# Performance work log

Measured on AMD Instinct MI355X. Metric: run time of the kernel, lower is better.

Reference implementation:

```python
import jax, jax.numpy as jnp
import numpy as np

B, S, D = 16, 2048, 768  # batch, padded subword length, roberta hidden dim


def setup_inputs() -> dict:
    key = jax.random.key(0)
    k1, k2 = jax.random.split(key)
    robert_embed = jax.random.normal(k1, (B, S, D), dtype=jnp.float32)
    # Non-decreasing per-row segment ids: contiguous runs of equal ids are the
    # subword spans that merge_list would average; singleton runs pass through.
    seg_ids = jnp.sort(jax.random.randint(k2, (B, S), 0, S, dtype=jnp.int32), axis=-1)
    return {"robert_embed": robert_embed, "seg_ids": seg_ids}


def reference(robert_embed, seg_ids):
    # Segment-mean gather/scatter: out[b, w] = mean_{p: seg_ids[b,p]==w} x[b, p]
    b, s, d = robert_embed.shape
    w = s  # output word slots (<= s); empty slots yield zeros
    flat_seg = (seg_ids + (w * jnp.arange(b, dtype=seg_ids.dtype))[:, None]).reshape(-1)
    x_flat = robert_embed.reshape(-1, d)
    sums = jax.ops.segment_sum(x_flat, flat_seg, num_segments=b * w)  # [b*w, d]
    counts = jax.ops.segment_sum(
        jnp.ones((b * s,), dtype=robert_embed.dtype), flat_seg, num_segments=b * w
    )
    out = sums / jnp.maximum(counts, 1)[:, None]
    return out.reshape(b, w, d)
```

## Files before the change

kernel.cpp:

```cpp
#include <hip/hip_runtime.h>

#define BB 16
#define SS 2048
#define DD 768
#define D4 (DD / 4)
#define SPB 16
#define BLOCKS_PER_ROW (SS / SPB)

typedef float vfloat4 __attribute__((ext_vector_type(4)));

__global__ __launch_bounds__(256) void seg_mean_v3(
    const float* __restrict__ x,
    const int*   __restrict__ seg,
    float*       __restrict__ out) {
    __shared__ int sLb[SPB + 1];

    int b  = blockIdx.x >> 7;
    int w0 = (blockIdx.x & (BLOCKS_PER_ROW - 1)) << 4;
    const int* srow = seg + (b << 11);

    if (threadIdx.x <= SPB) {
        int w  = w0 + threadIdx.x;
        int lo = 0, n = SS;
        while (n > 0) {
            int half = n >> 1;
            int mid  = lo + half;
            if (srow[mid] < w) { lo = mid + 1; n -= half + 1; }
            else               { n = half; }
        }
        sLb[threadIdx.x] = lo;
    }
    __syncthreads();

    int lane = threadIdx.x & 63;
    int wave = threadIdx.x >> 6;
    size_t rowBase = (size_t)(b << 11);

    for (int si = (wave << 2); si < (wave << 2) + 4; ++si) {
        int st = sLb[si];
        int c  = sLb[si + 1] - st;
        vfloat4* outp = (vfloat4*)(out + (rowBase + (size_t)(w0 + si)) * DD);

        if (c == 0) {
            vfloat4 z = (vfloat4){0.f, 0.f, 0.f, 0.f};
            __builtin_nontemporal_store(z, &outp[lane]);
            __builtin_nontemporal_store(z, &outp[lane + 64]);
            __builtin_nontemporal_store(z, &outp[lane + 128]);
            continue;
        }

        const vfloat4* xp = (const vfloat4*)(x + (rowBase + (size_t)st) * DD);
        vfloat4 a0 = xp[lane];
        vfloat4 a1 = xp[lane + 64];
        vfloat4 a2 = xp[lane + 128];
        for (int j = 1; j < c; ++j) {
            const vfloat4* xr = xp + (size_t)j * D4;
            a0 += xr[lane];
            a1 += xr[lane + 64];
            a2 += xr[lane + 128];
        }
        float inv = 1.0f / (float)c;
        a0 *= inv;
        a1 *= inv;
        a2 *= inv;
        __builtin_nontemporal_store(a0, &outp[lane]);
        __builtin_nontemporal_store(a1, &outp[lane + 64]);
        __builtin_nontemporal_store(a2, &outp[lane + 128]);
    }
}

extern "C" void kernel_launch(void* const* d_in, const int* in_sizes, int n_in,
                              void* d_out, int out_size, void* d_ws, size_t ws_size,
                              hipStream_t stream) {
    const float* x   = (const float*)d_in[0];
    const int*   seg = (const int*)d_in[1];
    float* out = (float*)d_out;

    int nBlocks = BB * BLOCKS_PER_ROW;
    seg_mean_v3<<<nBlocks, 256, 0, stream>>>(x, seg, out);
}
```

Baseline: 185.3 us.

## Stream input positions per block with register prefetch instead of per-output binary search

Switches from output-slot partitioning, where each block binary-searches segment bounds, to input-position partitioning. Each 192-thread block loads the full segment row into shared memory, owns 16 input positions, and walks runs that start in its chunk. It keeps an 8-deep register prefetch of input rows and writes the means plus zero-fill for empty slots in between. This is meant to remove serial dependent loads and global binary searches and to keep more loads in flight. The cost is copying the whole 2048-entry seg row per block, a serial scan with divergent branches, and uneven work when long runs or long zero gaps fall on one block.

```diff
diff --git a/kernel.cpp b/kernel.cpp
--- a/kernel.cpp
+++ b/kernel.cpp
@@ -3,70 +3,101 @@
 #define BB 16
 #define SS 2048
 #define DD 768
-#define D4 (DD / 4)
-#define SPB 16
-#define BLOCKS_PER_ROW (SS / SPB)
+#define D4 192
+#define P  16
+#define CPR (SS / P)
+#define PF 8
+#define NT 192
 
 typedef float vfloat4 __attribute__((ext_vector_type(4)));
 
-__global__ __launch_bounds__(256) void seg_mean_v3(
+__global__ __launch_bounds__(NT) void seg_mean_stream(
     const float* __restrict__ x,
     const int*   __restrict__ seg,
-    float*       __restrict__ out) {
-    __shared__ int sLb[SPB + 1];
+    float*       __restrict__ out)
+{
+    __shared__ __align__(16) int sseg[SS];
 
-    int b  = blockIdx.x >> 7;
-    int w0 = (blockIdx.x & (BLOCKS_PER_ROW - 1)) << 4;
-    const int* srow = seg + (b << 11);
+    const int b     = blockIdx.x >> 7;
+    const int chunk = blockIdx.x & (CPR - 1);
+    const int p0 = chunk * P;
+    const int p1 = p0 + P;
+    const int t  = threadIdx.x;
 
-    if (threadIdx.x <= SPB) {
-        int w  = w0 + threadIdx.x;
-        int lo = 0, n = SS;
-        while (n > 0) {
-            int half = n >> 1;
-            int mid  = lo + half;
-            if (srow[mid] < w) { lo = mid + 1; n -= half + 1; }
-            else               { n = half; }
+    {
+        const int4* s4 = (const int4*)(seg + (b << 11));
+        int4* l4 = (int4*)sseg;
+        #pragma unroll
+        for (int i = 0; i < 3; ++i) {
+            int idx = t + i * NT;
+            if (idx < SS / 4) l4[idx] = s4[idx];
         }
-        sLb[threadIdx.x] = lo;
     }
     __syncthreads();
 
-    int lane = threadIdx.x & 63;
-    int wave = threadIdx.x >> 6;
-    size_t rowBase = (size_t)(b << 11);
+    const int prev = (p0 == 0) ? -1 : sseg[p0 - 1];
+    int p = p0;
+    while (p < p1 && sseg[p] == prev) ++p;
+    if (p >= p1) return;
 
-    for (int si = (wave << 2); si < (wave << 2) + 4; ++si) {
-        int st = sLb[si];
-        int c  = sLb[si + 1] - st;
-        vfloat4* outp = (vfloat4*)(out + (rowBase + (size_t)(w0 + si)) * DD);
+    int pe = p1;
+    while (pe < SS && sseg[pe] == sseg[pe - 1]) ++pe;
 
-        if (c == 0) {
-            vfloat4 z = (vfloat4){0.f, 0.f, 0.f, 0.f};
-            __builtin_nontemporal_store(z, &outp[lane]);
-            __builtin_nontemporal_store(z, &outp[lane + 64]);
-            __builtin_nontemporal_store(z, &outp[lane + 128]);
-            continue;
-        }
+    const vfloat4* xrow = (const vfloat4*)(x + (((size_t)b) << 11) * DD);
+    float* outrow = out + (((size_t)b) << 11) * DD;
+    const vfloat4 z = (vfloat4){0.f, 0.f, 0.f, 0.f};
 
-        const vfloat4* xp = (const vfloat4*)(x + (rowBase + (size_t)st) * DD);
-        vfloat4 a0 = xp[lane];
-        vfloat4 a1 = xp[lane + 64];
-        vfloat4 a2 = xp[lane + 128];
-        for (int j = 1; j < c; ++j) {
-            const vfloat4* xr = xp + (size_t)j * D4;
-            a0 += xr[lane];
-            a1 += xr[lane + 64];
-            a2 += xr[lane + 128];
-        }
-        float inv = 1.0f / (float)c;
-        a0 *= inv;
-        a1 *= inv;
-        a2 *= inv;
-        __builtin_nontemporal_store(a0, &outp[lane]);
-        __builtin_nontemporal_store(a1, &outp[lane + 64]);
-        __builtin_nontemporal_store(a2, &outp[lane + 128]);
+    int runid = sseg[p];
+    for (int w = prev + 1; w < runid; ++w)
+        __builtin_nontemporal_store(z, (vfloat4*)(outrow + (size_t)w * DD) + t);
+
+    #define LDX(r) (xrow[(size_t)((r) < pe ? (r) : (pe - 1)) * D4 + t])
+    vfloat4 v0 = LDX(p + 0), v1 = LDX(p + 1), v2 = LDX(p + 2), v3 = LDX(p + 3);
+    vfloat4 v4 = LDX(p + 4), v5 = LDX(p + 5), v6 = LDX(p + 6), v7 = LDX(p + 7);
+
+    vfloat4 sum = z;
+    int cnt = 0;
+    bool done = false;
+
+    #define STEP(BUF) {                                                       \
+        vfloat4 cur = BUF;                                                    \
+        BUF = LDX(p + PF);                        \
+        sum += cur; ++cnt;                                                    \
+        int pn = p + 1;                                                       \
+        int sn = (pn < SS) ? sseg[pn] : -2;                                   \
+        if (sn != runid) {                                 \
+            vfloat4 m = sum * (1.0f / (float)cnt);                            \
+            __builtin_nontemporal_store(m,                                    \
+                (vfloat4*)(outrow + (size_t)runid * DD) + t);                 \
+            if (pn >= SS) {                      \
+                for (int w = runid + 1; w < SS; ++w)                          \
+                    __builtin_nontemporal_store(z,                            \
+                        (vfloat4*)(outrow + (size_t)w * DD) + t);             \
+                done = true;                                                  \
+            } else if (pn >= p1) {                     \
+                done = true;                                                  \
+            } else {                                \
+                for (int w = runid + 1; w < sn; ++w)                          \
+                    __builtin_nontemporal_store(z,                            \
+                        (vfloat4*)(outrow + (size_t)w * DD) + t);             \
+                runid = sn; sum = z; cnt = 0;                                 \
+            }                                                                 \
+        }                                                                     \
+        p = pn;                                                               \
     }
+
+    while (!done) {
+        STEP(v0); if (done) break;
+        STEP(v1); if (done) break;
+        STEP(v2); if (done) break;
+        STEP(v3); if (done) break;
+        STEP(v4); if (done) break;
+        STEP(v5); if (done) break;
+        STEP(v6); if (done) break;
+        STEP(v7); if (done) break;
+    }
+    #undef STEP
+    #undef LDX
 }
 
 extern "C" void kernel_launch(void* const* d_in, const int* in_sizes, int n_in,
@@ -76,6 +107,6 @@
     const int*   seg = (const int*)d_in[1];
     float* out = (float*)d_out;
 
-    int nBlocks = BB * BLOCKS_PER_ROW;
-    seg_mean_v3<<<nBlocks, 256, 0, stream>>>(x, seg, out);
+    int nBlocks = BB * CPR;
+    seg_mean_stream<<<nBlocks, NT, 0, stream>>>(x, seg, out);
 }
```

After: 184.8 us. Within noise of the previous version (-0.3%).

## Precompute segment boundaries in a separate kernel and prefetch first rows

Applied to the files above, without the earlier changes.

Splits the work into two kernels. The first loads each seg row into shared memory and binary-searches all segment boundaries into a workspace table. The main kernel reads those boundaries with vector loads and issues the first-row loads for all four of a wave's segments before accumulating, so more memory requests are in flight at once. The cost is an extra kernel launch and a workspace round trip.

```diff
diff --git a/kernel.cpp b/kernel.cpp
--- a/kernel.cpp
+++ b/kernel.cpp
@@ -3,69 +3,74 @@
 #define BB 16
 #define SS 2048
 #define DD 768
-#define D4 (DD / 4)
-#define SPB 16
-#define BLOCKS_PER_ROW (SS / SPB)
+#define D4 192
+#define MSTRIDE 2052
 
 typedef float vfloat4 __attribute__((ext_vector_type(4)));
 
-__global__ __launch_bounds__(256) void seg_mean_v3(
-    const float* __restrict__ x,
-    const int*   __restrict__ seg,
-    float*       __restrict__ out) {
-    __shared__ int sLb[SPB + 1];
-
-    int b  = blockIdx.x >> 7;
-    int w0 = (blockIdx.x & (BLOCKS_PER_ROW - 1)) << 4;
-    const int* srow = seg + (b << 11);
-
-    if (threadIdx.x <= SPB) {
-        int w  = w0 + threadIdx.x;
-        int lo = 0, n = SS;
-        while (n > 0) {
-            int half = n >> 1;
-            int mid  = lo + half;
-            if (srow[mid] < w) { lo = mid + 1; n -= half + 1; }
-            else               { n = half; }
-        }
-        sLb[threadIdx.x] = lo;
-    }
+__global__ __launch_bounds__(256) void build_meta(const int* __restrict__ seg,
+                                                  int* __restrict__ meta) {
+    __shared__ int srow[SS];
+    const int b = blockIdx.y;
+    const int4* g = (const int4*)(seg + b * SS);
+    for (int i = threadIdx.x; i < SS / 4; i += 256) ((int4*)srow)[i] = g[i];
     __syncthreads();
 
-    int lane = threadIdx.x & 63;
-    int wave = threadIdx.x >> 6;
-    size_t rowBase = (size_t)(b << 11);
+    int w = blockIdx.x * 256 + threadIdx.x;
+    if (w > SS) return;
+    int lo = 0, n = SS;
+    while (n > 0) {
+        int half = n >> 1, mid = lo + half;
+        if (srow[mid] < w) { lo = mid + 1; n -= half + 1; }
+        else               { n = half; }
+    }
+    meta[b * MSTRIDE + w] = lo;
+}
 
-    for (int si = (wave << 2); si < (wave << 2) + 4; ++si) {
-        int st = sLb[si];
-        int c  = sLb[si + 1] - st;
-        vfloat4* outp = (vfloat4*)(out + (rowBase + (size_t)(w0 + si)) * DD);
+__global__ __launch_bounds__(256) void seg_mean_v7(const float* __restrict__ x,
+                                                   const int* __restrict__ meta,
+                                                   float* __restrict__ out) {
+    const int b    = blockIdx.y;
+    const int lane = threadIdx.x & 63;
+    const int wave = threadIdx.x >> 6;
+    const int w0   = (blockIdx.x << 4) + (wave << 2);
 
+    const int* mp = meta + b * MSTRIDE + w0;
+    int4 m4 = *(const int4*)mp;
+    int  m5 = mp[4];
+    int st[5] = {m4.x, m4.y, m4.z, m4.w, m5};
+
+    const float* xbase = x + (size_t)b * SS * DD;
+    float*       obase = out + (size_t)b * SS * DD;
+
+    vfloat4 p[4][3];
+    #pragma unroll
+    for (int s = 0; s < 4; ++s) {
+        int r = (st[s] < st[s + 1]) ? st[s] : 0;
+        const vfloat4* xr = (const vfloat4*)(xbase + (size_t)r * DD);
+        p[s][0] = xr[lane]; p[s][1] = xr[lane + 64]; p[s][2] = xr[lane + 128];
+    }
+
+    #pragma unroll
+    for (int s = 0; s < 4; ++s) {
+        vfloat4* op = (vfloat4*)(obase + (size_t)(w0 + s) * DD);
+        int c = st[s + 1] - st[s];
         if (c == 0) {
-            vfloat4 z = (vfloat4){0.f, 0.f, 0.f, 0.f};
-            __builtin_nontemporal_store(z, &outp[lane]);
-            __builtin_nontemporal_store(z, &outp[lane + 64]);
-            __builtin_nontemporal_store(z, &outp[lane + 128]);
+            vfloat4 z = {0.f, 0.f, 0.f, 0.f};
+            __builtin_nontemporal_store(z, &op[lane]);
+            __builtin_nontemporal_store(z, &op[lane + 64]);
+            __builtin_nontemporal_store(z, &op[lane + 128]);
             continue;
         }
-
-        const vfloat4* xp = (const vfloat4*)(x + (rowBase + (size_t)st) * DD);
-        vfloat4 a0 = xp[lane];
-        vfloat4 a1 = xp[lane + 64];
-        vfloat4 a2 = xp[lane + 128];
+        vfloat4 a0 = p[s][0], a1 = p[s][1], a2 = p[s][2];
         for (int j = 1; j < c; ++j) {
-            const vfloat4* xr = xp + (size_t)j * D4;
-            a0 += xr[lane];
-            a1 += xr[lane + 64];
-            a2 += xr[lane + 128];
+            const vfloat4* xr = (const vfloat4*)(xbase + (size_t)(st[s] + j) * DD);
+            a0 += xr[lane]; a1 += xr[lane + 64]; a2 += xr[lane + 128];
         }
         float inv = 1.0f / (float)c;
-        a0 *= inv;
-        a1 *= inv;
-        a2 *= inv;
-        __builtin_nontemporal_store(a0, &outp[lane]);
-        __builtin_nontemporal_store(a1, &outp[lane + 64]);
-        __builtin_nontemporal_store(a2, &outp[lane + 128]);
+        __builtin_nontemporal_store(a0 * inv, &op[lane]);
+        __builtin_nontemporal_store(a1 * inv, &op[lane + 64]);
+        __builtin_nontemporal_store(a2 * inv, &op[lane + 128]);
     }
 }
 
@@ -74,8 +79,12 @@
                               hipStream_t stream) {
     const float* x   = (const float*)d_in[0];
     const int*   seg = (const int*)d_in[1];
-    float* out = (float*)d_out;
+    float* out  = (float*)d_out;
+    int*   meta = (int*)d_ws;
 
-    int nBlocks = BB * BLOCKS_PER_ROW;
-    seg_mean_v3<<<nBlocks, 256, 0, stream>>>(x, seg, out);
+    dim3 g0((SS + 1 + 255) / 256, BB);
+    build_meta<<<g0, 256, 0, stream>>>(seg, meta);
+
+    dim3 g1(SS / 16, BB);
+    seg_mean_v7<<<g1, 256, 0, stream>>>(x, meta, out);
 }
```

After: 184.4 us. Within noise of the previous version (-0.5%).
